# Performance work log

Measured on AMD Instinct MI355X. Metric: run time of the kernel, lower is better.

The kernel has to match this reference:

```python
import jax, jax.numpy as jnp
import numpy as np

N, C = 8192, 64

def setup_inputs() -> dict:
    key = jax.random.key(0)
    kA, kY = jax.random.split(key)
    A = jax.random.uniform(kA, (N, N), dtype=jnp.float32)
    Y = jax.random.normal(kY, (N, C), dtype=jnp.float32)
    return {"A": A, "Y": Y}

def reference(A, Y):
    # soft assignments
    Ys = jax.nn.softmax(Y, axis=1)                 # [n, C]
    # M[i, j] = Y_i^T A Y_j  (C x C); diag == total_ewc, strict-upper == pairwise ice
    M = jnp.einsum('ni,nm,mj->ij', Ys, A, Ys)      # two GEMMs, no n x n x C tensor
    total_ewc = jnp.diag(M)                        # [C]
    nwc = Ys.sum(axis=0)                           # [C]
    max_ewc = (nwc * (nwc - 1.0) + 1e-08) / 2.0
    cohesion = (total_ewc / max_ewc).sum()
    inter_cluster_edges = jnp.sum(jnp.triu(M, 1))  # sum_{i<j} Y_i^T A Y_j
    total_edges = A.sum()
    coupling = inter_cluster_edges / (total_edges + 1e-09)
    return -cohesion + coupling
```

## Files before the change

### kernel.cpp

```cpp
#include <hip/hip_runtime.h>
#include <hip/hip_bf16.h>

#define NN 8192
#define CC 64
#define KSPLIT 8
#define KCHUNK (NN / KSPLIT)
#define BK 64
#define NSTEPS (KCHUNK / BK)

typedef __bf16 bf16;
typedef __bf16 bf16x8 __attribute__((ext_vector_type(8)));
typedef float f32x4 __attribute__((ext_vector_type(4)));
typedef unsigned short us8 __attribute__((ext_vector_type(8)));

__global__ __launch_bounds__(256) void k1_softmax(const float* __restrict__ Yin,
                                                  float* __restrict__ Ys,
                                                  unsigned short* __restrict__ YsT,
                                                  float* __restrict__ nwc_part) {
    __shared__ float lds_t[64][65];
    __shared__ float nwc_lds[4][64];
    const int t = threadIdx.x;
    const int w = t >> 6, lane = t & 63;
    const int b = blockIdx.x;
    const int r0 = b * 64;
    float nwc_acc = 0.f;
    for (int it = 0; it < 16; ++it) {
        const int rl = it * 4 + w;
        const int row = r0 + rl;
        float y = Yin[row * CC + lane];
        float mx = y;
        #pragma unroll
        for (int m = 32; m >= 1; m >>= 1) mx = fmaxf(mx, __shfl_xor(mx, m, 64));
        float e = __expf(y - mx);
        float s = e;
        #pragma unroll
        for (int m = 32; m >= 1; m >>= 1) s += __shfl_xor(s, m, 64);
        float ys = e / s;
        Ys[row * CC + lane] = ys;
        lds_t[lane][rl] = ys;
        nwc_acc += ys;
    }
    nwc_lds[w][lane] = nwc_acc;
    __syncthreads();
    if (t < 64)
        nwc_part[b * 64 + t] = nwc_lds[0][t] + nwc_lds[1][t] + nwc_lds[2][t] + nwc_lds[3][t];
    const int c = t >> 2, q = t & 3;
    unsigned short tmp[16];
    #pragma unroll
    for (int i = 0; i < 16; ++i) {
        float v = lds_t[c][q * 16 + i];
        tmp[i] = __builtin_bit_cast(unsigned short, (__bf16)v);
    }
    us8* dst = (us8*)(&YsT[(size_t)c * NN + r0 + q * 16]);
    dst[0] = *(us8*)(&tmp[0]);
    dst[1] = *(us8*)(&tmp[8]);
}

__global__ __launch_bounds__(256) void k2_gemm(const float* __restrict__ A,
                                               const unsigned short* __restrict__ YsT,
                                               float* __restrict__ Bpart,
                                               float* __restrict__ edges_part) {
    __shared__ __align__(16) unsigned char lds[16384];
    __shared__ float ered[4];
    const int t = threadIdx.x;
    const int w = t >> 6, lane = t & 63;
    const int rb = blockIdx.x;
    const int kb = blockIdx.y;
    const int row0 = rb * 64;
    const int k0 = kb * KCHUNK;
    float esum = 0.f;
    f32x4 acc[4] = {};

    const int lq = lane >> 4;
    const int l15 = lane & 15;
    const int lrow = w * 16 + l15;

    for (int s = 0; s < NSTEPS; ++s) {
        const int kbase = k0 + s * BK;
        __syncthreads();
        #pragma unroll
        for (int p = 0; p < 4; ++p) {
            const int idx = p * 256 + t;
            const int r = idx >> 4;
            const int c4 = idx & 15;
            const float4 v = *(const float4*)(&A[(size_t)(row0 + r) * NN + kbase + c4 * 4]);
            esum += v.x + v.y + v.z + v.w;
            unsigned int lo = (unsigned int)__builtin_bit_cast(unsigned short, (__bf16)v.x)
                            | ((unsigned int)__builtin_bit_cast(unsigned short, (__bf16)v.y) << 16);
            unsigned int hi = (unsigned int)__builtin_bit_cast(unsigned short, (__bf16)v.z)
                            | ((unsigned int)__builtin_bit_cast(unsigned short, (__bf16)v.w) << 16);
            const int chunk = c4 >> 1;
            const int byteoff = r * 128 + (((chunk ^ (r & 7)) << 4)) + ((c4 & 1) << 3);
            *(uint2*)(&lds[byteoff]) = make_uint2(lo, hi);
        }
        #pragma unroll
        for (int p = 0; p < 2; ++p) {
            const int cid = p * 256 + t;
            const int cc = cid >> 3;
            const int ch = cid & 7;
            const float4 v = *(const float4*)(&YsT[(size_t)cc * NN + kbase + ch * 8]);
            *(float4*)(&lds[8192 + cc * 128 + (((ch ^ (cc & 7)) << 4))]) = v;
        }
        __syncthreads();
        #pragma unroll
        for (int kk = 0; kk < 2; ++kk) {
            const int chA = ((kk * 4 + lq) ^ (lrow & 7)) << 4;
            const bf16x8 a = *(const bf16x8*)(&lds[lrow * 128 + chA]);
            #pragma unroll
            for (int t4 = 0; t4 < 4; ++t4) {
                const int col = t4 * 16 + l15;
                const int chB = ((kk * 4 + lq) ^ (col & 7)) << 4;
                const bf16x8 bb = *(const bf16x8*)(&lds[8192 + col * 128 + chB]);
                acc[t4] = __builtin_amdgcn_mfma_f32_16x16x32_bf16(a, bb, acc[t4], 0, 0, 0);
            }
        }
    }
    const size_t base = ((size_t)kb * NN + row0) * CC;
    #pragma unroll
    for (int t4 = 0; t4 < 4; ++t4) {
        const int col = t4 * 16 + l15;
        #pragma unroll
        for (int r = 0; r < 4; ++r) {
            const int grow = w * 16 + lq * 4 + r;
            Bpart[base + (size_t)grow * CC + col] = acc[t4][r];
        }
    }
    #pragma unroll
    for (int m = 32; m >= 1; m >>= 1) esum += __shfl_xor(esum, m, 64);
    if (lane == 0) ered[w] = esum;
    __syncthreads();
    if (t == 0) edges_part[rb * KSPLIT + kb] = ered[0] + ered[1] + ered[2] + ered[3];
}

__global__ __launch_bounds__(256) void k3_mpart(const float* __restrict__ Bpart,
                                                const float* __restrict__ Ys,
                                                float* __restrict__ Mpart) {
    __shared__ float bl[4096];
    __shared__ float yl[4096];
    const int t = threadIdx.x;
    const int b = blockIdx.x;
    const int r0 = b * 64;
    for (int k = 0; k < 16; ++k) {
        const int e = k * 256 + t;
        const int i = e >> 6, c = e & 63;
        const size_t off = ((size_t)(r0 + i)) * CC + c;
        float s = 0.f;
        #pragma unroll
        for (int p = 0; p < KSPLIT; ++p) s += Bpart[(size_t)p * NN * CC + off];
        bl[e] = s;
        yl[e] = Ys[off];
    }
    __syncthreads();
    const int w = t >> 6, lane = t & 63;
    float acc[16];
    #pragma unroll
    for (int k = 0; k < 16; ++k) acc[k] = 0.f;
    for (int i = 0; i < 64; ++i) {
        const float bv = bl[i * 64 + lane];
        #pragma unroll
        for (int k = 0; k < 16; ++k)
            acc[k] += yl[i * 64 + 4 * k + w] * bv;
    }
    #pragma unroll
    for (int k = 0; k < 16; ++k)
        Mpart[(size_t)b * 4096 + k * 256 + t] = acc[k];
}

__global__ __launch_bounds__(256) void k4_reduce(const float* __restrict__ Mpart,
                                                 float* __restrict__ M) {
    const int e = blockIdx.x * 256 + threadIdx.x;
    float s = 0.f;
    for (int b = 0; b < 128; ++b) s += Mpart[(size_t)b * 4096 + e];
    M[e] = s;
}

__global__ __launch_bounds__(256) void k5_final(const float* __restrict__ M,
                                                const float* __restrict__ nwc_part,
                                                const float* __restrict__ edges_part,
                                                float* __restrict__ out) {
    __shared__ float red[256];
    const int t = threadIdx.x;
    float se = 0.f, st = 0.f, sc = 0.f;
    for (int i = t; i < 128 * KSPLIT; i += 256) se += edges_part[i];
    for (int e = t; e < 4096; e += 256) {
        const int c1 = e >> 6, c2 = e & 63;
        if (c2 > c1) st += M[e];
    }
    if (t < 64) {
        float nwc = 0.f;
        for (int b = 0; b < 128; ++b) nwc += nwc_part[b * 64 + t];
        const float me = (nwc * (nwc - 1.0f) + 1e-8f) * 0.5f;
        sc = M[t * 65] / me;
    }
    red[t] = se; __syncthreads();
    for (int s = 128; s >= 1; s >>= 1) { if (t < s) red[t] += red[t + s]; __syncthreads(); }
    const float tot_e = red[0]; __syncthreads();
    red[t] = st; __syncthreads();
    for (int s = 128; s >= 1; s >>= 1) { if (t < s) red[t] += red[t + s]; __syncthreads(); }
    const float tot_triu = red[0]; __syncthreads();
    red[t] = sc; __syncthreads();
    for (int s = 128; s >= 1; s >>= 1) { if (t < s) red[t] += red[t + s]; __syncthreads(); }
    const float cohesion = red[0];
    if (t == 0)
        out[0] = -cohesion + tot_triu / (tot_e + 1e-9f);
}

extern "C" void kernel_launch(void* const* d_in, const int* in_sizes, int n_in,
                              void* d_out, int out_size, void* d_ws, size_t ws_size,
                              hipStream_t stream) {
    const float* A   = (const float*)d_in[0];
    const float* Yin = (const float*)d_in[1];
    float* out = (float*)d_out;
    char* ws = (char*)d_ws;
    float*          Ys         = (float*)(ws + 0);
    unsigned short* YsT        = (unsigned short*)(ws + 2097152);
    float*          nwc_part   = (float*)(ws + 3145728);
    float*          edges_part = (float*)(ws + 3178496);
    float*          Bpart      = (float*)(ws + 4194304);
    float*          Mpart      = (float*)(ws + 20971520);
    float*          M          = (float*)(ws + 23068672);

    k1_softmax<<<128, 256, 0, stream>>>(Yin, Ys, YsT, nwc_part);
    k2_gemm<<<dim3(128, KSPLIT), 256, 0, stream>>>(A, YsT, Bpart, edges_part);
    k3_mpart<<<128, 256, 0, stream>>>(Bpart, Ys, Mpart);
    k4_reduce<<<16, 256, 0, stream>>>(Mpart, M);
    k5_final<<<1, 256, 0, stream>>>(M, nwc_part, edges_part, out);
}
```

Baseline: 107.2 us.

## Load GEMM operands directly into MFMA registers, drop LDS staging and barriers

The A×Ys GEMM kernel no longer stages A and YsT tiles through shared memory with two barriers per step. Each lane loads its A fragment straight from global memory in the MFMA operand layout, converts it to bf16 in registers, and prefetches the next step's A one iteration ahead. YsT fragments are read directly from global memory, likely hitting cache. This removes LDS traffic and synchronisation but makes A loads less coalesced (32-byte pieces per row per lane) and repeats YsT reads across waves.

After: 145.5 us. 35.7% more time.

```diff
diff --git a/kernel.cpp b/kernel.cpp
--- a/kernel.cpp
+++ b/kernel.cpp
@@ -60,7 +60,6 @@
                                                const unsigned short* __restrict__ YsT,
                                                float* __restrict__ Bpart,
                                                float* __restrict__ edges_part) {
-    __shared__ __align__(16) unsigned char lds[16384];
     __shared__ float ered[4];
     const int t = threadIdx.x;
     const int w = t >> 6, lane = t & 63;
@@ -68,53 +67,56 @@
     const int kb = blockIdx.y;
     const int row0 = rb * 64;
     const int k0 = kb * KCHUNK;
-    float esum = 0.f;
-    f32x4 acc[4] = {};
-
     const int lq = lane >> 4;
     const int l15 = lane & 15;
-    const int lrow = w * 16 + l15;
-
+
+    const float* pa = A + (size_t)(row0 + w * 16 + l15) * NN + k0 + lq * 8;
+    const unsigned short* pb0 = YsT + (size_t)l15 * NN + k0 + lq * 8;
+
+    f32x4 acc[4] = {};
+    float esum = 0.f;
+
+    float4 c0 = *(const float4*)(pa + 0);
+    float4 c1 = *(const float4*)(pa + 4);
+    float4 c2 = *(const float4*)(pa + 32);
+    float4 c3 = *(const float4*)(pa + 36);
+
+    #pragma unroll 2
     for (int s = 0; s < NSTEPS; ++s) {
-        const int kbase = k0 + s * BK;
-        __syncthreads();
-        #pragma unroll
-        for (int p = 0; p < 4; ++p) {
-            const int idx = p * 256 + t;
-            const int r = idx >> 4;
-            const int c4 = idx & 15;
-            const float4 v = *(const float4*)(&A[(size_t)(row0 + r) * NN + kbase + c4 * 4]);
-            esum += v.x + v.y + v.z + v.w;
-            unsigned int lo = (unsigned int)__builtin_bit_cast(unsigned short, (__bf16)v.x)
-                            | ((unsigned int)__builtin_bit_cast(unsigned short, (__bf16)v.y) << 16);
-            unsigned int hi = (unsigned int)__builtin_bit_cast(unsigned short, (__bf16)v.z)
-                            | ((unsigned int)__builtin_bit_cast(unsigned short, (__bf16)v.w) << 16);
-            const int chunk = c4 >> 1;
-            const int byteoff = r * 128 + (((chunk ^ (r & 7)) << 4)) + ((c4 & 1) << 3);
-            *(uint2*)(&lds[byteoff]) = make_uint2(lo, hi);
+        const int offn = ((s + 1 < NSTEPS) ? (s + 1) : s) * BK;
+        const float4 n0 = *(const float4*)(pa + offn + 0);
+        const float4 n1 = *(const float4*)(pa + offn + 4);
+        const float4 n2 = *(const float4*)(pa + offn + 32);
+        const float4 n3 = *(const float4*)(pa + offn + 36);
+
+        const int offb = s * BK;
+        bf16x8 b0[4], b1[4];
+        #pragma unroll
+        for (int t4 = 0; t4 < 4; ++t4) {
+            const unsigned short* pb = pb0 + (size_t)t4 * 16 * NN + offb;
+            b0[t4] = *(const bf16x8*)(pb);
+            b1[t4] = *(const bf16x8*)(pb + 32);
         }
-        #pragma unroll
-        for (int p = 0; p < 2; ++p) {
-            const int cid = p * 256 + t;
-            const int cc = cid >> 3;
-            const int ch = cid & 7;
-            const float4 v = *(const float4*)(&YsT[(size_t)cc * NN + kbase + ch * 8]);
-            *(float4*)(&lds[8192 + cc * 128 + (((ch ^ (cc & 7)) << 4))]) = v;
-        }
-        __syncthreads();
-        #pragma unroll
-        for (int kk = 0; kk < 2; ++kk) {
-            const int chA = ((kk * 4 + lq) ^ (lrow & 7)) << 4;
-            const bf16x8 a = *(const bf16x8*)(&lds[lrow * 128 + chA]);
-            #pragma unroll
-            for (int t4 = 0; t4 < 4; ++t4) {
-                const int col = t4 * 16 + l15;
-                const int chB = ((kk * 4 + lq) ^ (col & 7)) << 4;
-                const bf16x8 bb = *(const bf16x8*)(&lds[8192 + col * 128 + chB]);
-                acc[t4] = __builtin_amdgcn_mfma_f32_16x16x32_bf16(a, bb, acc[t4], 0, 0, 0);
-            }
-        }
-    }
+
+        esum += (c0.x + c0.y + c0.z + c0.w) + (c1.x + c1.y + c1.z + c1.w)
+              + (c2.x + c2.y + c2.z + c2.w) + (c3.x + c3.y + c3.z + c3.w);
+
+        bf16x8 a0, a1;
+        a0[0] = (__bf16)c0.x; a0[1] = (__bf16)c0.y; a0[2] = (__bf16)c0.z; a0[3] = (__bf16)c0.w;
+        a0[4] = (__bf16)c1.x; a0[5] = (__bf16)c1.y; a0[6] = (__bf16)c1.z; a0[7] = (__bf16)c1.w;
+        a1[0] = (__bf16)c2.x; a1[1] = (__bf16)c2.y; a1[2] = (__bf16)c2.z; a1[3] = (__bf16)c2.w;
+        a1[4] = (__bf16)c3.x; a1[5] = (__bf16)c3.y; a1[6] = (__bf16)c3.z; a1[7] = (__bf16)c3.w;
+
+        #pragma unroll
+        for (int t4 = 0; t4 < 4; ++t4)
+            acc[t4] = __builtin_amdgcn_mfma_f32_16x16x32_bf16(a0, b0[t4], acc[t4], 0, 0, 0);
+        #pragma unroll
+        for (int t4 = 0; t4 < 4; ++t4)
+            acc[t4] = __builtin_amdgcn_mfma_f32_16x16x32_bf16(a1, b1[t4], acc[t4], 0, 0, 0);
+
+        c0 = n0; c1 = n1; c2 = n2; c3 = n3;
+    }
+
     const size_t base = ((size_t)kb * NN + row0) * CC;
     #pragma unroll
     for (int t4 = 0; t4 < 4; ++t4) {
```

## Stage A and YsT tiles via direct global-to-LDS loads with fp32 A in LDS

Applied to the files above, without the earlier changes.

Replaces register-staged global loads of A and YsT with __builtin_amdgcn_global_load_lds, which copies 16-byte chunks straight into LDS using an XOR-swizzled source address. A now sits in LDS as fp32, and the bf16 conversion and edge-sum accumulation move to the MFMA operand read path. The aim is to cut VGPR traffic and load-issue overhead in the memory-bound A stream. The cost is double the LDS footprint for A and more LDS read bandwidth per step, and there is still no double buffering.

Result: slower. 132.4 us (+23.5%).

```diff
diff --git a/kernel.cpp b/kernel.cpp
--- a/kernel.cpp
+++ b/kernel.cpp
@@ -60,7 +60,8 @@
                                                const unsigned short* __restrict__ YsT,
                                                float* __restrict__ Bpart,
                                                float* __restrict__ edges_part) {
-    __shared__ __align__(16) unsigned char lds[16384];
+    __shared__ __align__(16) float ldsA[64 * 64];
+    __shared__ __align__(16) unsigned short ldsB[64 * 64];
     __shared__ float ered[4];
     const int t = threadIdx.x;
     const int w = t >> 6, lane = t & 63;
@@ -68,53 +69,58 @@
     const int kb = blockIdx.y;
     const int row0 = rb * 64;
     const int k0 = kb * KCHUNK;
+    const int lq = lane >> 4;
+    const int l15 = lane & 15;
+
+    const int ar  = lane >> 4;
+    const int ach = lane & 15;
+    const int bc  = lane >> 3;
+    const int bch = lane & 7;
+
     float esum = 0.f;
     f32x4 acc[4] = {};
-
-    const int lq = lane >> 4;
-    const int l15 = lane & 15;
-    const int lrow = w * 16 + l15;
 
     for (int s = 0; s < NSTEPS; ++s) {
         const int kbase = k0 + s * BK;
         __syncthreads();
         #pragma unroll
-        for (int p = 0; p < 4; ++p) {
-            const int idx = p * 256 + t;
-            const int r = idx >> 4;
-            const int c4 = idx & 15;
-            const float4 v = *(const float4*)(&A[(size_t)(row0 + r) * NN + kbase + c4 * 4]);
-            esum += v.x + v.y + v.z + v.w;
-            unsigned int lo = (unsigned int)__builtin_bit_cast(unsigned short, (__bf16)v.x)
-                            | ((unsigned int)__builtin_bit_cast(unsigned short, (__bf16)v.y) << 16);
-            unsigned int hi = (unsigned int)__builtin_bit_cast(unsigned short, (__bf16)v.z)
-                            | ((unsigned int)__builtin_bit_cast(unsigned short, (__bf16)v.w) << 16);
-            const int chunk = c4 >> 1;
-            const int byteoff = r * 128 + (((chunk ^ (r & 7)) << 4)) + ((c4 & 1) << 3);
-            *(uint2*)(&lds[byteoff]) = make_uint2(lo, hi);
-        }
-        #pragma unroll
-        for (int p = 0; p < 2; ++p) {
-            const int cid = p * 256 + t;
-            const int cc = cid >> 3;
-            const int ch = cid & 7;
-            const float4 v = *(const float4*)(&YsT[(size_t)cc * NN + kbase + ch * 8]);
-            *(float4*)(&lds[8192 + cc * 128 + (((ch ^ (cc & 7)) << 4))]) = v;
+        for (int p = 0; p < 16; ++p) {
+            const int r = p * 4 + ar;
+            const float* src = A + (size_t)(row0 + r) * NN + kbase + ((ach ^ (r & 7)) << 2);
+            __builtin_amdgcn_global_load_lds(
+                (const __attribute__((address_space(1))) unsigned int*)src,
+                (__attribute__((address_space(3))) unsigned int*)&ldsA[p * 256], 16, 0, 0);
+        }
+        #pragma unroll
+        for (int q = 0; q < 8; ++q) {
+            const int c = q * 8 + bc;
+            const unsigned short* src = YsT + (size_t)c * NN + kbase + ((bch ^ (c & 7)) << 3);
+            __builtin_amdgcn_global_load_lds(
+                (const __attribute__((address_space(1))) unsigned int*)src,
+                (__attribute__((address_space(3))) unsigned int*)&ldsB[q * 512], 16, 0, 0);
         }
         __syncthreads();
         #pragma unroll
         for (int kk = 0; kk < 2; ++kk) {
-            const int chA = ((kk * 4 + lq) ^ (lrow & 7)) << 4;
-            const bf16x8 a = *(const bf16x8*)(&lds[lrow * 128 + chA]);
+            const int r = w * 16 + l15;
+            const int cc = kk * 8 + lq * 2;
+            const int ch0 = cc ^ (r & 7);
+            const f32x4 fa0 = *(const f32x4*)&ldsA[r * 64 + (ch0 << 2)];
+            const f32x4 fa1 = *(const f32x4*)&ldsA[r * 64 + ((ch0 ^ 1) << 2)];
+            esum += (fa0[0] + fa0[1] + fa0[2] + fa0[3]) + (fa1[0] + fa1[1] + fa1[2] + fa1[3]);
+            bf16x8 a;
+            a[0] = (__bf16)fa0[0]; a[1] = (__bf16)fa0[1]; a[2] = (__bf16)fa0[2]; a[3] = (__bf16)fa0[3];
+            a[4] = (__bf16)fa1[0]; a[5] = (__bf16)fa1[1]; a[6] = (__bf16)fa1[2]; a[7] = (__bf16)fa1[3];
             #pragma unroll
             for (int t4 = 0; t4 < 4; ++t4) {
                 const int col = t4 * 16 + l15;
-                const int chB = ((kk * 4 + lq) ^ (col & 7)) << 4;
-                const bf16x8 bb = *(const bf16x8*)(&lds[8192 + col * 128 + chB]);
+                const int chB = (kk * 4 + lq) ^ (col & 7);
+                const bf16x8 bb = *(const bf16x8*)&ldsB[col * 64 + (chB << 3)];
                 acc[t4] = __builtin_amdgcn_mfma_f32_16x16x32_bf16(a, bb, acc[t4], 0, 0, 0);
             }
         }
     }
+
     const size_t base = ((size_t)kb * NN + row0) * CC;
     #pragma unroll
     for (int t4 = 0; t4 < 4; ++t4) {
```
